# Performance work log

Hardware: AMD Instinct MI355X
Metric: run time of the kernel (lower is better)

## Reference

```python
import jax, jax.numpy as jnp
import numpy as np

N_NODES = 20000


def _gcn_conv(x, edge_index, W, b):
    """PyG GCNConv: add self-loops, symmetric normalization, x @ W, scatter-add, + bias."""
    n = x.shape[0]
    loops = jnp.arange(n, dtype=edge_index.dtype)
    src = jnp.concatenate([edge_index[0], loops])  # [E+N]
    dst = jnp.concatenate([edge_index[1], loops])  # [E+N]
    # degree of target nodes (edge weight 1), self-loops guarantee deg >= 1
    deg = jax.ops.segment_sum(jnp.ones_like(dst, dtype=x.dtype), dst, num_segments=n)
    dinv = jax.lax.rsqrt(deg)
    norm = dinv[src] * dinv[dst]  # [E+N]
    h = x @ W  # [n, out] dense GEMM before aggregation (standard GCNConv ordering)
    msg = h[src] * norm[:, None]  # gather + scale over edges
    out = jax.ops.segment_sum(msg, dst, num_segments=n)  # scatter-add to targets
    return out + b


def setup_inputs() -> dict:
    key = jax.random.key(0)
    k = jax.random.split(key, 6)
    in_f, h_f, n_cls = 512, 512, 256
    x = jax.random.normal(k[0], (N_NODES, in_f), dtype=jnp.float32)
    edge_index = jax.random.randint(k[1], (2, 160000), 0, N_NODES, dtype=jnp.int64)
    W1 = jax.random.normal(k[2], (in_f, h_f), dtype=jnp.float32) * (1.0 / np.sqrt(in_f))
    b1 = jnp.zeros((h_f,), dtype=jnp.float32)
    W2 = jax.random.normal(k[3], (h_f, n_cls), dtype=jnp.float32) * (1.0 / np.sqrt(h_f))
    b2 = jnp.zeros((n_cls,), dtype=jnp.float32)
    return {"x": x, "edge_index": edge_index, "W1": W1, "b1": b1, "W2": W2, "b2": b2}


def reference(x, edge_index, W1, b1, W2, b2):
    h = jax.nn.relu(_gcn_conv(x, edge_index, W1, b1))
    h = jax.nn.relu(_gcn_conv(h, edge_index, W2, b2))
    # F.dropout in eval mode is identity; reference is deterministic eval-mode forward
    return h
```

## Files before the change

### kernel.cpp

```cpp
#include <hip/hip_runtime.h>


typedef __bf16 bf16x8 __attribute__((ext_vector_type(8)));
typedef float floatx4 __attribute__((ext_vector_type(4)));
typedef unsigned short ushort_t;
typedef unsigned int uint_t;

#define MAXD 32

__device__ inline ushort_t f2bf(float f) {
    unsigned u = __builtin_bit_cast(unsigned, f);
    unsigned r = (u + 0x7FFFu + ((u >> 16) & 1u)) >> 16;
    return (ushort_t)r;
}
__device__ inline float bf_lo(uint_t u) { return __builtin_bit_cast(float, u << 16); }
__device__ inline float bf_hi(uint_t u) { return __builtin_bit_cast(float, u & 0xFFFF0000u); }

__device__ inline void transpose_tile(const float* __restrict__ in,
                                      ushort_t* __restrict__ out,
                                      int K, int N, int k0, int n0,
                                      ushort_t (*tile)[33]) {
    int tx = threadIdx.x & 31, ty = threadIdx.x >> 5;
    for (int r = ty; r < 32; r += 8)
        tile[r][tx] = f2bf(in[(size_t)(k0 + r) * N + n0 + tx]);
    __syncthreads();
    for (int r = ty; r < 32; r += 8)
        out[(size_t)(n0 + r) * K + k0 + tx] = tile[tx][r];
}

__global__ __launch_bounds__(256) void prep_fused(
    const int* __restrict__ src, const int* __restrict__ dst,
    int* __restrict__ deg, int* __restrict__ col_ell,
    int* __restrict__ ovf_cnt, int* __restrict__ ovf, int e, int nb_e,
    const float* __restrict__ x, ushort_t* __restrict__ xb, long xcount, int nb_conv,
    const float* __restrict__ W1, ushort_t* __restrict__ w1t,
    const float* __restrict__ W2, ushort_t* __restrict__ w2t) {
    __shared__ ushort_t tile[32][33];
    int b = blockIdx.x;
    if (b < nb_e) {
        int i = b * 256 + threadIdx.x;
        if (i < e) {
            int s = src[i], d = dst[i];
            int slot = atomicAdd(&deg[d], 1);
            if (slot < MAXD) {
                col_ell[d * MAXD + slot] = s;
            } else {
                int k = atomicAdd(ovf_cnt, 1);
                ovf[2 * k] = d;
                ovf[2 * k + 1] = s;
            }
        }
        return;
    }
    b -= nb_e;
    if (b < nb_conv) {
        long i = ((long)b * 256 + threadIdx.x) * 4;
        if (i < xcount) {
            float4 v = *(const float4*)(x + i);
            ushort4 o = make_ushort4(f2bf(v.x), f2bf(v.y), f2bf(v.z), f2bf(v.w));
            *(ushort4*)(xb + i) = o;
        }
        return;
    }
    b -= nb_conv;
    if (b < 256) {
        transpose_tile(W1, w1t, 512, 512, (b >> 4) * 32, (b & 15) * 32, tile);
        return;
    }
    b -= 256;
    transpose_tile(W2, w2t, 512, 256, (b >> 3) * 32, (b & 7) * 32, tile);
}

__global__ __launch_bounds__(256) void gemm_mfma(
    const ushort_t* __restrict__ A, const ushort_t* __restrict__ BT,
    const float* __restrict__ dinv, ushort_t* __restrict__ C,
    int M, int N, int K, int nbx, int gemm_blocks, int scale,
    const int* __restrict__ deg, float* __restrict__ dinv_out, int n) {
    __shared__ __align__(16) ushort_t As[8192];
    __shared__ __align__(16) ushort_t Bs[8192];

    if ((int)blockIdx.x >= gemm_blocks) {
        int i = ((int)blockIdx.x - gemm_blocks) * 256 + threadIdx.x;
        if (i < n) dinv_out[i] = 1.0f / sqrtf((float)(deg[i] + 1));
        return;
    }

    const int bx = (int)blockIdx.x % nbx, by = (int)blockIdx.x / nbx;
    const int tid = threadIdx.x;
    const int w = tid >> 6, lane = tid & 63;
    const int q = lane >> 4, ml = lane & 15;
    const int wm = (w >> 1) * 64, wn = (w & 1) * 64;
    const int row0 = by * 128, col0 = bx * 128;

    const int rr = lane >> 3;
    const int gsw = (lane & 7) ^ (rr & 7);
    const ushort_t* ga[4];
    const ushort_t* gb[4];
    ushort_t* la[4];
    ushort_t* lb[4];
#pragma unroll
    for (int rp = 0; rp < 4; rp++) {
        int r = rp * 32 + w * 8 + rr;
        int gra = min(row0 + r, M - 1);
        ga[rp] = A + (size_t)gra * K + gsw * 8;
        gb[rp] = BT + (size_t)(col0 + r) * K + gsw * 8;
        la[rp] = As + rp * 2048 + w * 512;
        lb[rp] = Bs + rp * 2048 + w * 512;
    }

    const int sel = ml & 7;
    int aoff[2][4], boff[2][4];
#pragma unroll
    for (int st = 0; st < 2; st++)
#pragma unroll
        for (int i = 0; i < 4; i++) {
            int g = q + st * 4;
            aoff[st][i] = (wm + i * 16 + ml) * 64 + ((g ^ sel) << 3);
            boff[st][i] = (wn + i * 16 + ml) * 64 + ((g ^ sel) << 3);
        }

    floatx4 acc[4][4];
#pragma unroll
    for (int i = 0; i < 4; i++)
#pragma unroll
        for (int j = 0; j < 4; j++) acc[i][j] = (floatx4)0.0f;

    for (int kt = 0; kt < K; kt += 64) {
#pragma unroll
        for (int rp = 0; rp < 4; rp++) {
            __builtin_amdgcn_global_load_lds(
                (const __attribute__((address_space(1))) unsigned*)ga[rp],
                (__attribute__((address_space(3))) unsigned*)la[rp], 16, 0, 0);
            __builtin_amdgcn_global_load_lds(
                (const __attribute__((address_space(1))) unsigned*)gb[rp],
                (__attribute__((address_space(3))) unsigned*)lb[rp], 16, 0, 0);
            ga[rp] += 64; gb[rp] += 64;
        }
        __syncthreads();
#pragma unroll
        for (int st = 0; st < 2; st++) {
            bf16x8 af[4], bfr[4];
#pragma unroll
            for (int i = 0; i < 4; i++) {
                af[i] = *(const bf16x8*)(As + aoff[st][i]);
                bfr[i] = *(const bf16x8*)(Bs + boff[st][i]);
            }
#pragma unroll
            for (int i = 0; i < 4; i++)
#pragma unroll
                for (int j = 0; j < 4; j++)
                    acc[i][j] = __builtin_amdgcn_mfma_f32_16x16x32_bf16(
                        af[i], bfr[j], acc[i][j], 0, 0, 0);
        }
        __syncthreads();
    }

#pragma unroll
    for (int i = 0; i < 4; i++) {
        int rbase = row0 + wm + i * 16 + q * 4;
        float pd[4];
#pragma unroll
        for (int r = 0; r < 4; r++)
            pd[r] = (scale && rbase + r < M) ? dinv[rbase + r] : 1.0f;
#pragma unroll
        for (int j = 0; j < 4; j++) {
            int gc = col0 + wn + j * 16 + ml;
#pragma unroll
            for (int r = 0; r < 4; r++) {
                int gr = rbase + r;
                if (gr < M) C[(size_t)gr * N + gc] = f2bf(pd[r] * acc[i][j][r]);
            }
        }
    }
}

__global__ __launch_bounds__(128) void aggregate1(const uint2* __restrict__ g,
                                                  const int* __restrict__ deg,
                                                  const int* __restrict__ col_ell,
                                                  const int* __restrict__ ovf_cnt,
                                                  const int* __restrict__ ovf,
                                                  const float* __restrict__ dinv,
                                                  const float* __restrict__ bias,
                                                  uint2* __restrict__ out) {
    const int d = blockIdx.x, t = threadIdx.x;
    const int cnt = min(deg[d], MAXD);
    const float pd = dinv[d];
    const size_t base = (size_t)d * 128 + t;
    const int* cm = col_ell + (size_t)d * MAXD;

    const int lane = t & 63;
    int cv = 0;
    float dv = 0.0f;
    if (lane < MAXD && lane < cnt) {
        cv = cm[lane];
        dv = dinv[cv];
    }
    float4 b = *(const float4*)(bias + t * 4);

    uint2 us = g[base];
    float a0 = pd * bf_lo(us.x), a1 = pd * bf_hi(us.x);
    float a2 = pd * bf_lo(us.y), a3 = pd * bf_hi(us.y);

    for (int e0 = 0; e0 < cnt; e0 += 8) {
        uint2 u[8];
        float ps[8];
#pragma unroll
        for (int j = 0; j < 8; j++) {
            int s = __shfl(cv, e0 + j);
            ps[j] = __shfl(dv, e0 + j);
            u[j] = g[(size_t)s * 128 + t];
        }
#pragma unroll
        for (int j = 0; j < 8; j++) {
            a0 = fmaf(ps[j], bf_lo(u[j].x), a0);
            a1 = fmaf(ps[j], bf_hi(u[j].x), a1);
            a2 = fmaf(ps[j], bf_lo(u[j].y), a2);
            a3 = fmaf(ps[j], bf_hi(u[j].y), a3);
        }
    }
    int nov = *ovf_cnt;
    for (int k = 0; k < nov; k++) {
        if (ovf[2 * k] == d) {
            int s = ovf[2 * k + 1];
            float ps = dinv[s];
            uint2 u = g[(size_t)s * 128 + t];
            a0 = fmaf(ps, bf_lo(u.x), a0);
            a1 = fmaf(ps, bf_hi(u.x), a1);
            a2 = fmaf(ps, bf_lo(u.y), a2);
            a3 = fmaf(ps, bf_hi(u.y), a3);
        }
    }
    float o0 = fmaxf(fmaf(pd, a0, b.x), 0.0f);
    float o1 = fmaxf(fmaf(pd, a1, b.y), 0.0f);
    float o2 = fmaxf(fmaf(pd, a2, b.z), 0.0f);
    float o3 = fmaxf(fmaf(pd, a3, b.w), 0.0f);
    uint2 o;
    o.x = (uint_t)f2bf(o0) | ((uint_t)f2bf(o1) << 16);
    o.y = (uint_t)f2bf(o2) | ((uint_t)f2bf(o3) << 16);
    out[base] = o;
}

__global__ __launch_bounds__(64) void aggregate2(const uint2* __restrict__ g,
                                                 const int* __restrict__ deg,
                                                 const int* __restrict__ col_ell,
                                                 const int* __restrict__ ovf_cnt,
                                                 const int* __restrict__ ovf,
                                                 const float* __restrict__ dinv,
                                                 const float* __restrict__ bias,
                                                 float* __restrict__ out) {
    const int d = blockIdx.x, t = threadIdx.x;
    const int cnt = min(deg[d], MAXD);
    const float pd = dinv[d];
    const size_t base = (size_t)d * 64 + t;
    const int* cm = col_ell + (size_t)d * MAXD;

    int cv = 0;
    float wv = 0.0f;
    if (t < MAXD && t < cnt) {
        cv = cm[t];
        wv = 1.0f;
    }
    float4 b = *(const float4*)(bias + t * 4);

    uint2 us = g[base];
    float a0 = bf_lo(us.x), a1 = bf_hi(us.x);
    float a2 = bf_lo(us.y), a3 = bf_hi(us.y);

    for (int e0 = 0; e0 < cnt; e0 += 8) {
        uint2 u[8];
        float ws[8];
#pragma unroll
        for (int j = 0; j < 8; j++) {
            int s = __shfl(cv, e0 + j);
            ws[j] = __shfl(wv, e0 + j);
            u[j] = g[(size_t)s * 64 + t];
        }
#pragma unroll
        for (int j = 0; j < 8; j++) {
            a0 = fmaf(ws[j], bf_lo(u[j].x), a0);
            a1 = fmaf(ws[j], bf_hi(u[j].x), a1);
            a2 = fmaf(ws[j], bf_lo(u[j].y), a2);
            a3 = fmaf(ws[j], bf_hi(u[j].y), a3);
        }
    }
    int nov = *ovf_cnt;
    for (int k = 0; k < nov; k++) {
        if (ovf[2 * k] == d) {
            uint2 u = g[(size_t)ovf[2 * k + 1] * 64 + t];
            a0 += bf_lo(u.x); a1 += bf_hi(u.x);
            a2 += bf_lo(u.y); a3 += bf_hi(u.y);
        }
    }
    float4 o;
    o.x = fmaxf(fmaf(pd, a0, b.x), 0.0f);
    o.y = fmaxf(fmaf(pd, a1, b.y), 0.0f);
    o.z = fmaxf(fmaf(pd, a2, b.z), 0.0f);
    o.w = fmaxf(fmaf(pd, a3, b.w), 0.0f);
    *(float4*)(out + (size_t)d * 256 + t * 4) = o;
}

extern "C" void kernel_launch(void* const* d_in, const int* in_sizes, int n_in,
                              void* d_out, int out_size, void* d_ws, size_t ws_size,
                              hipStream_t stream) {
    const float* x  = (const float*)d_in[0];
    const int*   ei = (const int*)d_in[1];
    const float* W1 = (const float*)d_in[2];
    const float* b1 = (const float*)d_in[3];
    const float* W2 = (const float*)d_in[4];
    const float* b2 = (const float*)d_in[5];
    float* out = (float*)d_out;

    const int FIN = 512, FH = 512, FOUT = 256;
    const int n = in_sizes[0] / FIN;
    const int e = in_sizes[1] / 2;
    const int* src = ei;
    const int* dst = ei + e;

    auto align_up = [](size_t v) { return (v + 255) & ~(size_t)255; };
    char* w = (char*)d_ws;
    int*      deg     = (int*)w;
    int*      ovf_cnt = deg + n;
    w += align_up((size_t)(n + 1) * 4);
    float*    dinv    = (float*)w;    w += align_up((size_t)n * 4);
    int*      col_ell = (int*)w;      w += align_up((size_t)n * MAXD * 4);
    int*      ovf     = (int*)w;      w += align_up((size_t)2048 * 4);
    ushort_t* xb      = (ushort_t*)w; w += align_up((size_t)n * FIN * 2);
    ushort_t* w1t     = (ushort_t*)w; w += align_up((size_t)FH * FIN * 2);
    ushort_t* w2t     = (ushort_t*)w; w += align_up((size_t)FOUT * FH * 2);
    ushort_t* g       = (ushort_t*)w; w += align_up((size_t)n * FH * 2);
    ushort_t* h1b     = (ushort_t*)w; w += align_up((size_t)n * FH * 2);

    const int nb_n = (n + 255) / 256;
    const int nb_e = (e + 255) / 256;
    const long xcount = (long)n * FIN;
    const int nb_conv = (int)((xcount / 4 + 255) / 256);

    hipMemsetAsync(deg, 0, (size_t)(n + 1) * 4, stream);

    prep_fused<<<nb_e + nb_conv + 256 + 128, 256, 0, stream>>>(
        src, dst, deg, col_ell, ovf_cnt, ovf, e, nb_e,
        x, xb, xcount, nb_conv, W1, w1t, W2, w2t);

    const int mb = (n + 127) / 128;
    {
        int gemm_blocks = (FH / 128) * mb;
        gemm_mfma<<<gemm_blocks + nb_n, 256, 0, stream>>>(
            xb, w1t, nullptr, g, n, FH, FIN, FH / 128, gemm_blocks, 0,
            deg, dinv, n);
    }
    aggregate1<<<n, 128, 0, stream>>>((const uint2*)g, deg, col_ell, ovf_cnt,
                                      ovf, dinv, b1, (uint2*)h1b);
    {
        int gemm_blocks = (FOUT / 128) * mb;
        gemm_mfma<<<gemm_blocks, 256, 0, stream>>>(
            h1b, w2t, dinv, g, n, FOUT, FH, FOUT / 128, gemm_blocks, 1,
            nullptr, nullptr, 0);
    }
    aggregate2<<<n, 64, 0, stream>>>((const uint2*)g, deg, col_ell, ovf_cnt,
                                     ovf, dinv, b2, out);

    (void)ws_size; (void)n_in; (void)out_size;
}
```

Baseline: 193.2 us.

## Fuse layer-1 aggregation into the layer-2 GEMM A-tile producer

Removes the separate aggregate1 kernel and the h1b intermediate. A new gemm2_fused kernel builds each 64x64 bf16 A tile on the fly by gathering neighbor rows of g, applying the normalization, bias and ReLU, and writing the result into swizzled LDS. B tiles stream in through global_load_lds. This saves a full n x 512 bf16 round trip through HBM and one kernel launch. In exchange, the irregular gather is serialized inside the GEMM k-loop behind barriers, and the grid is only about 313 blocks, so latency hiding and load balance could suffer.

```diff
diff --git a/kernel.cpp b/kernel.cpp
--- a/kernel.cpp
+++ b/kernel.cpp
@@ -7,6 +7,7 @@
 typedef unsigned int uint_t;
 
 #define MAXD 32
+#define CAP 40
 
 __device__ inline ushort_t f2bf(float f) {
     unsigned u = __builtin_bit_cast(unsigned, f);
@@ -15,6 +16,9 @@
 }
 __device__ inline float bf_lo(uint_t u) { return __builtin_bit_cast(float, u << 16); }
 __device__ inline float bf_hi(uint_t u) { return __builtin_bit_cast(float, u & 0xFFFF0000u); }
+__device__ inline uint_t pk2(float lo, float hi) {
+    return (uint_t)f2bf(lo) | ((uint_t)f2bf(hi) << 16);
+}
 
 __device__ inline void transpose_tile(const float* __restrict__ in,
                                       ushort_t* __restrict__ out,
@@ -73,8 +77,8 @@
 
 __global__ __launch_bounds__(256) void gemm_mfma(
     const ushort_t* __restrict__ A, const ushort_t* __restrict__ BT,
-    const float* __restrict__ dinv, ushort_t* __restrict__ C,
-    int M, int N, int K, int nbx, int gemm_blocks, int scale,
+    ushort_t* __restrict__ C,
+    int M, int N, int K, int nbx, int gemm_blocks,
     const int* __restrict__ deg, float* __restrict__ dinv_out, int n) {
     __shared__ __align__(16) ushort_t As[8192];
     __shared__ __align__(16) ushort_t Bs[8192];
@@ -158,86 +162,199 @@
 #pragma unroll
     for (int i = 0; i < 4; i++) {
         int rbase = row0 + wm + i * 16 + q * 4;
-        float pd[4];
-#pragma unroll
-        for (int r = 0; r < 4; r++)
-            pd[r] = (scale && rbase + r < M) ? dinv[rbase + r] : 1.0f;
 #pragma unroll
         for (int j = 0; j < 4; j++) {
             int gc = col0 + wn + j * 16 + ml;
 #pragma unroll
             for (int r = 0; r < 4; r++) {
                 int gr = rbase + r;
-                if (gr < M) C[(size_t)gr * N + gc] = f2bf(pd[r] * acc[i][j][r]);
-            }
-        }
-    }
-}
-
-__global__ __launch_bounds__(128) void aggregate1(const uint2* __restrict__ g,
-                                                  const int* __restrict__ deg,
-                                                  const int* __restrict__ col_ell,
-                                                  const int* __restrict__ ovf_cnt,
-                                                  const int* __restrict__ ovf,
-                                                  const float* __restrict__ dinv,
-                                                  const float* __restrict__ bias,
-                                                  uint2* __restrict__ out) {
-    const int d = blockIdx.x, t = threadIdx.x;
-    const int cnt = min(deg[d], MAXD);
-    const float pd = dinv[d];
-    const size_t base = (size_t)d * 128 + t;
-    const int* cm = col_ell + (size_t)d * MAXD;
-
-    const int lane = t & 63;
-    int cv = 0;
-    float dv = 0.0f;
-    if (lane < MAXD && lane < cnt) {
-        cv = cm[lane];
-        dv = dinv[cv];
-    }
-    float4 b = *(const float4*)(bias + t * 4);
-
-    uint2 us = g[base];
-    float a0 = pd * bf_lo(us.x), a1 = pd * bf_hi(us.x);
-    float a2 = pd * bf_lo(us.y), a3 = pd * bf_hi(us.y);
-
-    for (int e0 = 0; e0 < cnt; e0 += 8) {
-        uint2 u[8];
-        float ps[8];
-#pragma unroll
-        for (int j = 0; j < 8; j++) {
-            int s = __shfl(cv, e0 + j);
-            ps[j] = __shfl(dv, e0 + j);
-            u[j] = g[(size_t)s * 128 + t];
-        }
-#pragma unroll
-        for (int j = 0; j < 8; j++) {
-            a0 = fmaf(ps[j], bf_lo(u[j].x), a0);
-            a1 = fmaf(ps[j], bf_hi(u[j].x), a1);
-            a2 = fmaf(ps[j], bf_lo(u[j].y), a2);
-            a3 = fmaf(ps[j], bf_hi(u[j].y), a3);
-        }
-    }
-    int nov = *ovf_cnt;
-    for (int k = 0; k < nov; k++) {
-        if (ovf[2 * k] == d) {
-            int s = ovf[2 * k + 1];
-            float ps = dinv[s];
-            uint2 u = g[(size_t)s * 128 + t];
-            a0 = fmaf(ps, bf_lo(u.x), a0);
-            a1 = fmaf(ps, bf_hi(u.x), a1);
-            a2 = fmaf(ps, bf_lo(u.y), a2);
-            a3 = fmaf(ps, bf_hi(u.y), a3);
-        }
-    }
-    float o0 = fmaxf(fmaf(pd, a0, b.x), 0.0f);
-    float o1 = fmaxf(fmaf(pd, a1, b.y), 0.0f);
-    float o2 = fmaxf(fmaf(pd, a2, b.z), 0.0f);
-    float o3 = fmaxf(fmaf(pd, a3, b.w), 0.0f);
-    uint2 o;
-    o.x = (uint_t)f2bf(o0) | ((uint_t)f2bf(o1) << 16);
-    o.y = (uint_t)f2bf(o2) | ((uint_t)f2bf(o3) << 16);
-    out[base] = o;
+                if (gr < M) C[(size_t)gr * N + gc] = f2bf(acc[i][j][r]);
+            }
+        }
+    }
+}
+
+__global__ __launch_bounds__(256, 2) void gemm2_fused(
+    const ushort_t* __restrict__ g,
+    const ushort_t* __restrict__ BT,
+    const int* __restrict__ deg, const int* __restrict__ col_ell,
+    const int* __restrict__ ovf_cnt, const int* __restrict__ ovf,
+    const float* __restrict__ dinv, const float* __restrict__ b1,
+    ushort_t* __restrict__ g2, int M) {
+    __shared__ __align__(16) ushort_t As[64 * 64];
+    __shared__ __align__(16) ushort_t Bs[256 * 64];
+    __shared__ int   cols_s[64][CAP];
+    __shared__ float ps_s[64][CAP];
+    __shared__ float b1_s[512];
+    __shared__ short cnt_s[64];
+
+    const int tid = threadIdx.x;
+    const int w = tid >> 6, lane = tid & 63;
+    const int q = lane >> 4, ml = lane & 15;
+    const int wn = w * 64;
+    const int row0 = (int)blockIdx.x * 64;
+
+    for (int i = tid; i < 512; i += 256) b1_s[i] = b1[i];
+    {
+        int r = tid >> 2, jj = tid & 3;
+        int rg = min(row0 + r, M - 1);
+        int cnt = min(deg[rg], MAXD);
+        float pd = dinv[rg];
+        if (jj == 0) {
+            cols_s[r][0] = rg;
+            ps_s[r][0] = pd;
+            cnt_s[r] = (short)(cnt + 1);
+        }
+        const int* cm = col_ell + (size_t)rg * MAXD;
+        for (int j = jj; j < CAP - 1; j += 4) {
+            bool vld = j < cnt;
+            int c = vld ? cm[j] : rg;
+            cols_s[r][j + 1] = c;
+            ps_s[r][j + 1] = vld ? dinv[c] : 0.0f;
+        }
+    }
+    const int nov = *ovf_cnt;
+
+    const int rr = lane >> 3;
+    const int gsw = (lane & 7) ^ (rr & 7);
+    const ushort_t* gb[8];
+    ushort_t* lb[8];
+#pragma unroll
+    for (int rp = 0; rp < 8; rp++) {
+        gb[rp] = BT + (size_t)(rp * 32 + w * 8 + rr) * 512 + gsw * 8;
+        lb[rp] = Bs + rp * 2048 + w * 512;
+    }
+
+    const int sel = ml & 7;
+    int aoff[2][4], boff[2][4];
+#pragma unroll
+    for (int st = 0; st < 2; st++)
+#pragma unroll
+        for (int i = 0; i < 4; i++) {
+            int gg = q + st * 4;
+            aoff[st][i] = (i * 16 + ml) * 64 + ((gg ^ sel) << 3);
+            boff[st][i] = (wn + i * 16 + ml) * 64 + ((gg ^ sel) << 3);
+        }
+
+    floatx4 acc[4][4];
+#pragma unroll
+    for (int i = 0; i < 4; i++)
+#pragma unroll
+        for (int j = 0; j < 4; j++) acc[i][j] = (floatx4)0.0f;
+
+    const int ar = tid >> 3;
+    const int kg = tid & 7;
+
+    __syncthreads();
+
+    for (int kt = 0; kt < 512; kt += 64) {
+#pragma unroll
+        for (int rp = 0; rp < 8; rp++) {
+            __builtin_amdgcn_global_load_lds(
+                (const __attribute__((address_space(1))) unsigned*)gb[rp],
+                (__attribute__((address_space(3))) unsigned*)lb[rp], 16, 0, 0);
+            gb[rp] += 64;
+        }
+
+        const ushort_t* gk = g + kt + kg * 8;
+#pragma unroll
+        for (int p = 0; p < 2; p++) {
+            const int r = ar + p * 32;
+            const int cntR = (int)cnt_s[r];
+            const float pdr = ps_s[r][0];
+            float a[8];
+#pragma unroll
+            for (int k = 0; k < 8; k++) a[k] = 0.0f;
+            for (int e0 = 0; e0 < cntR; e0 += 8) {
+                uint4 u[8];
+                float ps[8];
+#pragma unroll
+                for (int j = 0; j < 8; j++) {
+                    int s = cols_s[r][e0 + j];
+                    ps[j] = ps_s[r][e0 + j];
+                    u[j] = *(const uint4*)(gk + (size_t)s * 512);
+                }
+#pragma unroll
+                for (int j = 0; j < 8; j++) {
+                    a[0] = fmaf(ps[j], bf_lo(u[j].x), a[0]);
+                    a[1] = fmaf(ps[j], bf_hi(u[j].x), a[1]);
+                    a[2] = fmaf(ps[j], bf_lo(u[j].y), a[2]);
+                    a[3] = fmaf(ps[j], bf_hi(u[j].y), a[3]);
+                    a[4] = fmaf(ps[j], bf_lo(u[j].z), a[4]);
+                    a[5] = fmaf(ps[j], bf_hi(u[j].z), a[5]);
+                    a[6] = fmaf(ps[j], bf_lo(u[j].w), a[6]);
+                    a[7] = fmaf(ps[j], bf_hi(u[j].w), a[7]);
+                }
+            }
+            for (int k2 = 0; k2 < nov; k2++) {
+                if (ovf[2 * k2] == cols_s[r][0]) {
+                    int s = ovf[2 * k2 + 1];
+                    float ps = dinv[s];
+                    uint4 u = *(const uint4*)(gk + (size_t)s * 512);
+                    a[0] = fmaf(ps, bf_lo(u.x), a[0]);
+                    a[1] = fmaf(ps, bf_hi(u.x), a[1]);
+                    a[2] = fmaf(ps, bf_lo(u.y), a[2]);
+                    a[3] = fmaf(ps, bf_hi(u.y), a[3]);
+                    a[4] = fmaf(ps, bf_lo(u.z), a[4]);
+                    a[5] = fmaf(ps, bf_hi(u.z), a[5]);
+                    a[6] = fmaf(ps, bf_lo(u.w), a[6]);
+                    a[7] = fmaf(ps, bf_hi(u.w), a[7]);
+                }
+            }
+            float4 bv0 = *(const float4*)(b1_s + kt + kg * 8);
+            float4 bv1 = *(const float4*)(b1_s + kt + kg * 8 + 4);
+            float h0 = fmaxf(fmaf(pdr, a[0], bv0.x), 0.0f);
+            float h1 = fmaxf(fmaf(pdr, a[1], bv0.y), 0.0f);
+            float h2 = fmaxf(fmaf(pdr, a[2], bv0.z), 0.0f);
+            float h3 = fmaxf(fmaf(pdr, a[3], bv0.w), 0.0f);
+            float h4 = fmaxf(fmaf(pdr, a[4], bv1.x), 0.0f);
+            float h5 = fmaxf(fmaf(pdr, a[5], bv1.y), 0.0f);
+            float h6 = fmaxf(fmaf(pdr, a[6], bv1.z), 0.0f);
+            float h7 = fmaxf(fmaf(pdr, a[7], bv1.w), 0.0f);
+            uint4 U;
+            U.x = pk2(h0, h1);
+            U.y = pk2(h2, h3);
+            U.z = pk2(h4, h5);
+            U.w = pk2(h6, h7);
+            *(uint4*)(As + r * 64 + ((kg ^ (r & 7)) << 3)) = U;
+        }
+        __syncthreads();
+
+#pragma unroll
+        for (int st = 0; st < 2; st++) {
+            bf16x8 af[4], bfr[4];
+#pragma unroll
+            for (int i = 0; i < 4; i++) {
+                af[i] = *(const bf16x8*)(As + aoff[st][i]);
+                bfr[i] = *(const bf16x8*)(Bs + boff[st][i]);
+            }
+#pragma unroll
+            for (int i = 0; i < 4; i++)
+#pragma unroll
+                for (int j = 0; j < 4; j++)
+                    acc[i][j] = __builtin_amdgcn_mfma_f32_16x16x32_bf16(
+                        af[i], bfr[j], acc[i][j], 0, 0, 0);
+        }
+        __syncthreads();
+    }
+
+#pragma unroll
+    for (int i = 0; i < 4; i++) {
+        int rbase = row0 + i * 16 + q * 4;
+        float pd4[4];
+#pragma unroll
+        for (int r = 0; r < 4; r++)
+            pd4[r] = (rbase + r < M) ? dinv[rbase + r] : 1.0f;
+#pragma unroll
+        for (int j = 0; j < 4; j++) {
+            int gc = wn + j * 16 + ml;
+#pragma unroll
+            for (int r = 0; r < 4; r++) {
+                int gr = rbase + r;
+                if (gr < M) g2[(size_t)gr * 256 + gc] = f2bf(pd4[r] * acc[i][j][r]);
+            }
+        }
+    }
 }
 
 __global__ __launch_bounds__(64) void aggregate2(const uint2* __restrict__ g,
@@ -328,7 +445,7 @@
     ushort_t* w1t     = (ushort_t*)w; w += align_up((size_t)FH * FIN * 2);
     ushort_t* w2t     = (ushort_t*)w; w += align_up((size_t)FOUT * FH * 2);
     ushort_t* g       = (ushort_t*)w; w += align_up((size_t)n * FH * 2);
-    ushort_t* h1b     = (ushort_t*)w; w += align_up((size_t)n * FH * 2);
+    ushort_t* g2      = (ushort_t*)w; w += align_up((size_t)n * FH * 2);
 
     const int nb_n = (n + 255) / 256;
     const int nb_e = (e + 255) / 256;
@@ -341,22 +458,16 @@
         src, dst, deg, col_ell, ovf_cnt, ovf, e, nb_e,
         x, xb, xcount, nb_conv, W1, w1t, W2, w2t);
 
-    const int mb = (n + 127) / 128;
     {
+        const int mb = (n + 127) / 128;
         int gemm_blocks = (FH / 128) * mb;
         gemm_mfma<<<gemm_blocks + nb_n, 256, 0, stream>>>(
-            xb, w1t, nullptr, g, n, FH, FIN, FH / 128, gemm_blocks, 0,
-            deg, dinv, n);
-    }
-    aggregate1<<<n, 128, 0, stream>>>((const uint2*)g, deg, col_ell, ovf_cnt,
-                                      ovf, dinv, b1, (uint2*)h1b);
-    {
-        int gemm_blocks = (FOUT / 128) * mb;
-        gemm_mfma<<<gemm_blocks, 256, 0, stream>>>(
-            h1b, w2t, dinv, g, n, FOUT, FH, FOUT / 128, gemm_blocks, 1,
-            nullptr, nullptr, 0);
-    }
-    aggregate2<<<n, 64, 0, stream>>>((const uint2*)g, deg, col_ell, ovf_cnt,
+            xb, w1t, g, n, FH, FIN, FH / 128, gemm_blocks, deg, dinv, n);
+    }
+    gemm2_fused<<<(n + 63) / 64, 256, 0, stream>>>(
+        g, w2t, deg, col_ell, ovf_cnt, ovf, dinv, b1, g2, n);
+
+    aggregate2<<<n, 64, 0, stream>>>((const uint2*)g2, deg, col_ell, ovf_cnt,
                                      ovf, dinv, b2, out);
 
     (void)ws_size; (void)n_in; (void)out_size;
```

Result: slower. 199.0 us (+3.0%).

## Fuse layer-1 aggregation with layer-2 GEMM in one kernel

Applied to the files above, without the earlier changes.

Replaces the separate aggregate1 kernel and second gemm_mfma launch with a single kernel. Each 512-thread block aggregates 32 destination rows of layer-1 features into swizzled shared memory, then multiplies them by W2 with MFMA and writes the dinv-scaled result. This removes the round trip of the 20000x512 bf16 hidden activations through global memory and one launch. The cost is a narrower GEMM tile with B fragments read straight from global memory on every block, and more shared memory per block, which may lower occupancy.

```diff
diff --git a/kernel.cpp b/kernel.cpp
--- a/kernel.cpp
+++ b/kernel.cpp
@@ -15,6 +15,9 @@
 }
 __device__ inline float bf_lo(uint_t u) { return __builtin_bit_cast(float, u << 16); }
 __device__ inline float bf_hi(uint_t u) { return __builtin_bit_cast(float, u & 0xFFFF0000u); }
+__device__ inline uint_t pk2(float lo, float hi) {
+    return (uint_t)f2bf(lo) | ((uint_t)f2bf(hi) << 16);
+}
 
 __device__ inline void transpose_tile(const float* __restrict__ in,
                                       ushort_t* __restrict__ out,
@@ -73,8 +76,8 @@
 
 __global__ __launch_bounds__(256) void gemm_mfma(
     const ushort_t* __restrict__ A, const ushort_t* __restrict__ BT,
-    const float* __restrict__ dinv, ushort_t* __restrict__ C,
-    int M, int N, int K, int nbx, int gemm_blocks, int scale,
+    ushort_t* __restrict__ C,
+    int M, int N, int K, int nbx, int gemm_blocks,
     const int* __restrict__ deg, float* __restrict__ dinv_out, int n) {
     __shared__ __align__(16) ushort_t As[8192];
     __shared__ __align__(16) ushort_t Bs[8192];
@@ -158,86 +161,170 @@
 #pragma unroll
     for (int i = 0; i < 4; i++) {
         int rbase = row0 + wm + i * 16 + q * 4;
-        float pd[4];
-#pragma unroll
-        for (int r = 0; r < 4; r++)
-            pd[r] = (scale && rbase + r < M) ? dinv[rbase + r] : 1.0f;
 #pragma unroll
         for (int j = 0; j < 4; j++) {
             int gc = col0 + wn + j * 16 + ml;
 #pragma unroll
             for (int r = 0; r < 4; r++) {
                 int gr = rbase + r;
-                if (gr < M) C[(size_t)gr * N + gc] = f2bf(pd[r] * acc[i][j][r]);
-            }
-        }
-    }
-}
-
-__global__ __launch_bounds__(128) void aggregate1(const uint2* __restrict__ g,
-                                                  const int* __restrict__ deg,
-                                                  const int* __restrict__ col_ell,
-                                                  const int* __restrict__ ovf_cnt,
-                                                  const int* __restrict__ ovf,
-                                                  const float* __restrict__ dinv,
-                                                  const float* __restrict__ bias,
-                                                  uint2* __restrict__ out) {
-    const int d = blockIdx.x, t = threadIdx.x;
-    const int cnt = min(deg[d], MAXD);
-    const float pd = dinv[d];
-    const size_t base = (size_t)d * 128 + t;
-    const int* cm = col_ell + (size_t)d * MAXD;
-
-    const int lane = t & 63;
-    int cv = 0;
-    float dv = 0.0f;
-    if (lane < MAXD && lane < cnt) {
-        cv = cm[lane];
-        dv = dinv[cv];
-    }
-    float4 b = *(const float4*)(bias + t * 4);
-
-    uint2 us = g[base];
-    float a0 = pd * bf_lo(us.x), a1 = pd * bf_hi(us.x);
-    float a2 = pd * bf_lo(us.y), a3 = pd * bf_hi(us.y);
-
-    for (int e0 = 0; e0 < cnt; e0 += 8) {
-        uint2 u[8];
-        float ps[8];
-#pragma unroll
-        for (int j = 0; j < 8; j++) {
-            int s = __shfl(cv, e0 + j);
-            ps[j] = __shfl(dv, e0 + j);
-            u[j] = g[(size_t)s * 128 + t];
-        }
-#pragma unroll
-        for (int j = 0; j < 8; j++) {
-            a0 = fmaf(ps[j], bf_lo(u[j].x), a0);
-            a1 = fmaf(ps[j], bf_hi(u[j].x), a1);
-            a2 = fmaf(ps[j], bf_lo(u[j].y), a2);
-            a3 = fmaf(ps[j], bf_hi(u[j].y), a3);
-        }
-    }
-    int nov = *ovf_cnt;
-    for (int k = 0; k < nov; k++) {
-        if (ovf[2 * k] == d) {
-            int s = ovf[2 * k + 1];
-            float ps = dinv[s];
-            uint2 u = g[(size_t)s * 128 + t];
-            a0 = fmaf(ps, bf_lo(u.x), a0);
-            a1 = fmaf(ps, bf_hi(u.x), a1);
-            a2 = fmaf(ps, bf_lo(u.y), a2);
-            a3 = fmaf(ps, bf_hi(u.y), a3);
-        }
-    }
-    float o0 = fmaxf(fmaf(pd, a0, b.x), 0.0f);
-    float o1 = fmaxf(fmaf(pd, a1, b.y), 0.0f);
-    float o2 = fmaxf(fmaf(pd, a2, b.z), 0.0f);
-    float o3 = fmaxf(fmaf(pd, a3, b.w), 0.0f);
-    uint2 o;
-    o.x = (uint_t)f2bf(o0) | ((uint_t)f2bf(o1) << 16);
-    o.y = (uint_t)f2bf(o2) | ((uint_t)f2bf(o3) << 16);
-    out[base] = o;
+                if (gr < M) C[(size_t)gr * N + gc] = f2bf(acc[i][j][r]);
+            }
+        }
+    }
+}
+
+__global__ __launch_bounds__(512, 4) void agg1gemm2(
+    const ushort_t* __restrict__ g,
+    const ushort_t* __restrict__ BT,
+    const int* __restrict__ deg, const int* __restrict__ col_ell,
+    const int* __restrict__ ovf_cnt, const int* __restrict__ ovf,
+    const float* __restrict__ dinv, const float* __restrict__ b1,
+    ushort_t* __restrict__ g2, int M) {
+    __shared__ __align__(16) ushort_t As[32 * 512];
+
+    const int tid = threadIdx.x;
+    const int w = tid >> 6, lane = tid & 63;
+    const int q = lane >> 4, ml = lane & 15;
+    const int wm = (w >> 2) * 16, wn = (w & 3) * 64;
+    const int row0 = (int)blockIdx.x * 32;
+
+    const int nov = *ovf_cnt;
+    const int c = lane;
+
+    float4 bv0 = *(const float4*)(b1 + c * 8);
+    float4 bv1 = *(const float4*)(b1 + c * 8 + 4);
+
+#pragma unroll
+    for (int p = 0; p < 4; p++) {
+        const int lr = p * 8 + w;
+        const int rP = min(row0 + lr, M - 1);
+        const int cnt = min(deg[rP], MAXD);
+        const float pd = dinv[rP];
+
+        int cv = rP;
+        float dv = 0.0f;
+        if (lane < cnt) {
+            cv = col_ell[(size_t)rP * MAXD + lane];
+            dv = dinv[cv];
+        }
+
+        uint4 us = *(const uint4*)(g + (size_t)rP * 512 + c * 8);
+        float a0 = pd * bf_lo(us.x), a1 = pd * bf_hi(us.x);
+        float a2 = pd * bf_lo(us.y), a3 = pd * bf_hi(us.y);
+        float a4 = pd * bf_lo(us.z), a5 = pd * bf_hi(us.z);
+        float a6 = pd * bf_lo(us.w), a7 = pd * bf_hi(us.w);
+
+        for (int e0 = 0; e0 < cnt; e0 += 8) {
+            uint4 u[8];
+            float ps[8];
+#pragma unroll
+            for (int j = 0; j < 8; j++) {
+                int s = __shfl(cv, e0 + j);
+                ps[j] = __shfl(dv, e0 + j);
+                u[j] = *(const uint4*)(g + (size_t)s * 512 + c * 8);
+            }
+#pragma unroll
+            for (int j = 0; j < 8; j++) {
+                a0 = fmaf(ps[j], bf_lo(u[j].x), a0);
+                a1 = fmaf(ps[j], bf_hi(u[j].x), a1);
+                a2 = fmaf(ps[j], bf_lo(u[j].y), a2);
+                a3 = fmaf(ps[j], bf_hi(u[j].y), a3);
+                a4 = fmaf(ps[j], bf_lo(u[j].z), a4);
+                a5 = fmaf(ps[j], bf_hi(u[j].z), a5);
+                a6 = fmaf(ps[j], bf_lo(u[j].w), a6);
+                a7 = fmaf(ps[j], bf_hi(u[j].w), a7);
+            }
+        }
+        for (int k2 = 0; k2 < nov; k2++) {
+            if (ovf[2 * k2] == rP) {
+                int sI = ovf[2 * k2 + 1];
+                float ps = dinv[sI];
+                uint4 u = *(const uint4*)(g + (size_t)sI * 512 + c * 8);
+                a0 = fmaf(ps, bf_lo(u.x), a0);
+                a1 = fmaf(ps, bf_hi(u.x), a1);
+                a2 = fmaf(ps, bf_lo(u.y), a2);
+                a3 = fmaf(ps, bf_hi(u.y), a3);
+                a4 = fmaf(ps, bf_lo(u.z), a4);
+                a5 = fmaf(ps, bf_hi(u.z), a5);
+                a6 = fmaf(ps, bf_lo(u.w), a6);
+                a7 = fmaf(ps, bf_hi(u.w), a7);
+            }
+        }
+        float h0 = fmaxf(fmaf(pd, a0, bv0.x), 0.0f);
+        float h1 = fmaxf(fmaf(pd, a1, bv0.y), 0.0f);
+        float h2 = fmaxf(fmaf(pd, a2, bv0.z), 0.0f);
+        float h3 = fmaxf(fmaf(pd, a3, bv0.w), 0.0f);
+        float h4 = fmaxf(fmaf(pd, a4, bv1.x), 0.0f);
+        float h5 = fmaxf(fmaf(pd, a5, bv1.y), 0.0f);
+        float h6 = fmaxf(fmaf(pd, a6, bv1.z), 0.0f);
+        float h7 = fmaxf(fmaf(pd, a7, bv1.w), 0.0f);
+        uint4 U;
+        U.x = pk2(h0, h1);
+        U.y = pk2(h2, h3);
+        U.z = pk2(h4, h5);
+        U.w = pk2(h6, h7);
+        int pos = (c & ~7) | ((c & 7) ^ (lr & 7));
+        *(uint4*)(As + lr * 512 + pos * 8) = U;
+    }
+
+    const ushort_t* bp[4];
+#pragma unroll
+    for (int j = 0; j < 4; j++)
+        bp[j] = BT + (size_t)(wn + j * 16 + ml) * 512 + q * 8;
+
+    bf16x8 bfr[2][4];
+#pragma unroll
+    for (int st = 0; st < 2; st++)
+#pragma unroll
+        for (int j = 0; j < 4; j++)
+            bfr[st][j] = *(const bf16x8*)(bp[j] + st * 32);
+
+    __syncthreads();
+
+    const int sel = ml & 7;
+    int aoffb[2];
+#pragma unroll
+    for (int st = 0; st < 2; st++)
+        aoffb[st] = (wm + ml) * 512 + (((st * 4 + q) ^ sel) << 3);
+
+    floatx4 accm[4];
+#pragma unroll
+    for (int j = 0; j < 4; j++) accm[j] = (floatx4)0.0f;
+
+    for (int kt = 0; kt < 8; kt++) {
+        bf16x8 nb[2][4];
+        if (kt < 7) {
+#pragma unroll
+            for (int st = 0; st < 2; st++)
+#pragma unroll
+                for (int j = 0; j < 4; j++)
+                    nb[st][j] = *(const bf16x8*)(bp[j] + (kt + 1) * 64 + st * 32);
+        }
+#pragma unroll
+        for (int st = 0; st < 2; st++) {
+            bf16x8 af = *(const bf16x8*)(As + aoffb[st] + kt * 64);
+#pragma unroll
+            for (int j = 0; j < 4; j++)
+                accm[j] = __builtin_amdgcn_mfma_f32_16x16x32_bf16(
+                    af, bfr[st][j], accm[j], 0, 0, 0);
+        }
+#pragma unroll
+        for (int st = 0; st < 2; st++)
+#pragma unroll
+            for (int j = 0; j < 4; j++) bfr[st][j] = nb[st][j];
+    }
+
+#pragma unroll
+    for (int rg = 0; rg < 4; rg++) {
+        int grow = row0 + wm + q * 4 + rg;
+        float pd = (grow < M) ? dinv[grow] : 1.0f;
+#pragma unroll
+        for (int j = 0; j < 4; j++) {
+            int gcx = wn + j * 16 + ml;
+            if (grow < M)
+                g2[(size_t)grow * 256 + gcx] = f2bf(pd * accm[j][rg]);
+        }
+    }
 }
 
 __global__ __launch_bounds__(64) void aggregate2(const uint2* __restrict__ g,
@@ -328,7 +415,7 @@
     ushort_t* w1t     = (ushort_t*)w; w += align_up((size_t)FH * FIN * 2);
     ushort_t* w2t     = (ushort_t*)w; w += align_up((size_t)FOUT * FH * 2);
     ushort_t* g       = (ushort_t*)w; w += align_up((size_t)n * FH * 2);
-    ushort_t* h1b     = (ushort_t*)w; w += align_up((size_t)n * FH * 2);
+    ushort_t* g2      = (ushort_t*)w; w += align_up((size_t)n * FOUT * 2);
 
     const int nb_n = (n + 255) / 256;
     const int nb_e = (e + 255) / 256;
@@ -341,22 +428,16 @@
         src, dst, deg, col_ell, ovf_cnt, ovf, e, nb_e,
         x, xb, xcount, nb_conv, W1, w1t, W2, w2t);
 
-    const int mb = (n + 127) / 128;
     {
+        const int mb = (n + 127) / 128;
         int gemm_blocks = (FH / 128) * mb;
         gemm_mfma<<<gemm_blocks + nb_n, 256, 0, stream>>>(
-            xb, w1t, nullptr, g, n, FH, FIN, FH / 128, gemm_blocks, 0,
-            deg, dinv, n);
-    }
-    aggregate1<<<n, 128, 0, stream>>>((const uint2*)g, deg, col_ell, ovf_cnt,
-                                      ovf, dinv, b1, (uint2*)h1b);
-    {
-        int gemm_blocks = (FOUT / 128) * mb;
-        gemm_mfma<<<gemm_blocks, 256, 0, stream>>>(
-            h1b, w2t, dinv, g, n, FOUT, FH, FOUT / 128, gemm_blocks, 1,
-            nullptr, nullptr, 0);
-    }
-    aggregate2<<<n, 64, 0, stream>>>((const uint2*)g, deg, col_ell, ovf_cnt,
+            xb, w1t, g, n, FH, FIN, FH / 128, gemm_blocks, deg, dinv, n);
+    }
+    agg1gemm2<<<(n + 31) / 32, 512, 0, stream>>>(
+        g, w2t, deg, col_ell, ovf_cnt, ovf, dinv, b1, g2, n);
+
+    aggregate2<<<n, 64, 0, stream>>>((const uint2*)g2, deg, col_ell, ovf_cnt,
                                      ovf, dinv, b2, out);
 
     (void)ws_size; (void)n_in; (void)out_size;
```

After: 208.3 us. +7.8%, slower.
